# Kernel tuning notes

Measured on AMD Instinct MI355X. Metric: run time of the kernel, lower is better.

The kernel has to match this reference:

```python
import jax, jax.numpy as jnp
import numpy as np

N = 10000
E = 160000
DIMS = [512, 512, 512, 256]  # in -> hidden -> hidden -> out (num_layers=3)
EPS = 1e-12  # F.normalize default eps


def _sage_layer(x, edge_index, Wl, b, Wr):
    # PyG SAGEConv (mean aggr, normalize=True):
    # out = lin_l(mean_{j in N(i)} x_j) + lin_r(x_i), then L2-normalize rows.
    src = edge_index[0]
    dst = edge_index[1]
    msg = x[src]  # [E, d] gather of source-node features
    agg = jax.ops.segment_sum(msg, dst, num_segments=N)  # [N, d]
    cnt = jax.ops.segment_sum(jnp.ones((E,), x.dtype), dst, num_segments=N)
    mean = agg / jnp.maximum(cnt, 1.0)[:, None]
    out = mean @ Wl.T + b + x @ Wr.T
    norm = jnp.sqrt(jnp.sum(out * out, axis=-1, keepdims=True))
    return out / jnp.maximum(norm, EPS)


def setup_inputs() -> dict:
    key = jax.random.key(0)
    ks = jax.random.split(key, 2 + 3 * len(DIMS))
    x = jax.random.normal(ks[0], (N, DIMS[0]), dtype=jnp.float32)
    edge_index = jax.random.randint(ks[1], (2, E), 0, N, dtype=jnp.int64)
    inp = {"x": x, "edge_index": edge_index}
    k = 2
    for i in range(len(DIMS) - 1):
        din, dout = DIMS[i], DIMS[i + 1]
        s = 1.0 / np.sqrt(din)
        inp[f"Wl{i}"] = jax.random.uniform(ks[k], (dout, din), jnp.float32, -s, s); k += 1
        inp[f"b{i}"] = jax.random.uniform(ks[k], (dout,), jnp.float32, -s, s); k += 1
        inp[f"Wr{i}"] = jax.random.uniform(ks[k], (dout, din), jnp.float32, -s, s); k += 1
    return inp


def reference(x, edge_index, Wl0, b0, Wr0, Wl1, b1, Wr1, Wl2, b2, Wr2):
    params = [(Wl0, b0, Wr0), (Wl1, b1, Wr1), (Wl2, b2, Wr2)]
    for Wl, b, Wr in params:
        x = _sage_layer(x, edge_index, Wl, b, Wr)
        x = jax.nn.relu(x)
        # F.dropout(training=False) is identity at inference
    return x
```

## Files before the change

### kernel.cpp

```cpp
#include <hip/hip_runtime.h>

#define NN 10000

typedef __attribute__((ext_vector_type(8))) short short8;
typedef __attribute__((ext_vector_type(4))) float f32x4;

__device__ __forceinline__ ushort f2b(float f) {
    union { float f; uint32_t u; } v; v.f = f;
    uint32_t u = v.u;
    return (ushort)((u + 0x7fffu + ((u >> 16) & 1u)) >> 16);
}
__device__ __forceinline__ uint packbf(float a, float b) {
    return (uint)f2b(a) | ((uint)f2b(b) << 16);
}
__device__ __forceinline__ float blo(uint u) {
    union { uint u; float f; } v; v.u = u << 16; return v.f;
}
__device__ __forceinline__ float bhi(uint u) {
    union { uint u; float f; } v; v.u = u & 0xffff0000u; return v.f;
}

__global__ __launch_bounds__(256) void zero_int(int* __restrict__ p, int n) {
    int i = blockIdx.x * 256 + threadIdx.x;
    if (i < n) p[i] = 0;
}

__global__ __launch_bounds__(256) void count_dst(const int* __restrict__ dst,
                                                 int* __restrict__ counts, int E) {
    int i = blockIdx.x * 256 + threadIdx.x;
    if (i < E) atomicAdd(&counts[dst[i]], 1);
}

__global__ __launch_bounds__(1024) void scan_build(const int* __restrict__ counts,
                                                   int* __restrict__ offsets,
                                                   int* __restrict__ cursor,
                                                   float* __restrict__ inv_cnt, int n) {
    __shared__ int part[1024];
    int tid = threadIdx.x;
    int per = (n + 1023) / 1024;
    int base = tid * per;
    int s = 0;
    for (int i = 0; i < per; i++) { int idx = base + i; if (idx < n) s += counts[idx]; }
    part[tid] = s;
    __syncthreads();
    for (int off = 1; off < 1024; off <<= 1) {
        int v = (tid >= off) ? part[tid - off] : 0;
        __syncthreads();
        part[tid] += v;
        __syncthreads();
    }
    int run = (tid > 0) ? part[tid - 1] : 0;
    for (int i = 0; i < per; i++) {
        int idx = base + i;
        if (idx < n) {
            int c = counts[idx];
            offsets[idx] = run;
            cursor[idx]  = run;
            inv_cnt[idx] = 1.0f / fmaxf((float)c, 1.0f);
            run += c;
        }
    }
}

__global__ __launch_bounds__(256) void scatter_edges(const int* __restrict__ src,
                                                     const int* __restrict__ dst,
                                                     int* __restrict__ cursor,
                                                     int* __restrict__ sorted_src, int E) {
    int i = blockIdx.x * 256 + threadIdx.x;
    if (i < E) {
        int p = atomicAdd(&cursor[dst[i]], 1);
        sorted_src[p] = src[i];
    }
}

__global__ __launch_bounds__(256) void cvt_x(const float* __restrict__ in,
                                             ushort* __restrict__ xcat, int n4) {
    int i = blockIdx.x * 256 + threadIdx.x;
    if (i >= n4) return;
    int idx = i * 4;
    int node = idx >> 9;
    int col  = idx & 511;
    float4 v = *(const float4*)(in + (size_t)node * 512 + col);
    uint2 p;
    p.x = packbf(v.x, v.y);
    p.y = packbf(v.z, v.w);
    *(uint2*)(xcat + (size_t)node * 1024 + 512 + col) = p;
}

__global__ __launch_bounds__(256) void cvt_w(const float* __restrict__ Wl,
                                             const float* __restrict__ Wr,
                                             ushort* __restrict__ out, int n4) {
    int i = blockIdx.x * 256 + threadIdx.x;
    if (i >= n4) return;
    int idx = i * 4;
    int row = idx >> 10;
    int col = idx & 1023;
    const float* src = (col < 512) ? (Wl + (size_t)row * 512 + col)
                                   : (Wr + (size_t)row * 512 + col - 512);
    float4 v = *(const float4*)src;
    uint2 p;
    p.x = packbf(v.x, v.y);
    p.y = packbf(v.z, v.w);
    *(uint2*)(out + idx) = p;
}

__global__ __launch_bounds__(256) void agg_mean(ushort* __restrict__ xcat,
                                                const int* __restrict__ offsets,
                                                const int* __restrict__ counts,
                                                const int* __restrict__ sorted_src,
                                                const float* __restrict__ inv_cnt, int n) {
    int wave = threadIdx.x >> 6;
    int lane = threadIdx.x & 63;
    int node = blockIdx.x * 4 + wave;
    if (node >= n) return;
    int start = offsets[node];
    int cnt   = counts[node];
    float inv = inv_cnt[node];

    const uint* xr = (const uint*)xcat + 256;
    int l4 = lane * 4;

    float acc[8];
#pragma unroll
    for (int k = 0; k < 8; k++) acc[k] = 0.f;

    int e = 0;
    for (; e + 4 <= cnt; e += 4) {
        int s0 = sorted_src[start + e + 0];
        int s1 = sorted_src[start + e + 1];
        int s2 = sorted_src[start + e + 2];
        int s3 = sorted_src[start + e + 3];
        uint4 v0 = *(const uint4*)(xr + (size_t)s0 * 512 + l4);
        uint4 v1 = *(const uint4*)(xr + (size_t)s1 * 512 + l4);
        uint4 v2 = *(const uint4*)(xr + (size_t)s2 * 512 + l4);
        uint4 v3 = *(const uint4*)(xr + (size_t)s3 * 512 + l4);
#define ACC8(v) do { \
        acc[0] += blo(v.x); acc[1] += bhi(v.x); \
        acc[2] += blo(v.y); acc[3] += bhi(v.y); \
        acc[4] += blo(v.z); acc[5] += bhi(v.z); \
        acc[6] += blo(v.w); acc[7] += bhi(v.w); } while (0)
        ACC8(v0); ACC8(v1); ACC8(v2); ACC8(v3);
    }
    for (; e < cnt; e++) {
        int s0 = sorted_src[start + e];
        uint4 v0 = *(const uint4*)(xr + (size_t)s0 * 512 + l4);
        ACC8(v0);
    }
#undef ACC8

    uint4 o;
    o.x = packbf(acc[0] * inv, acc[1] * inv);
    o.y = packbf(acc[2] * inv, acc[3] * inv);
    o.z = packbf(acc[4] * inv, acc[5] * inv);
    o.w = packbf(acc[6] * inv, acc[7] * inv);
    *(uint4*)(xcat + (size_t)node * 1024 + lane * 8) = o;
}

__global__ __launch_bounds__(256) void gemm_mfma(const ushort* __restrict__ A,
                                                 const ushort* __restrict__ B,
                                                 float* __restrict__ C,
                                                 int M, int Nn) {
    __shared__ ushort Asl[64 * 32];
    __shared__ ushort Bsl[128 * 32];
    const int tid  = threadIdx.x;
    const int w    = tid >> 6;
    const int lane = tid & 63;
    const int bm = blockIdx.y * 64, bn = blockIdx.x * 128;
    const int wm = (w & 1) * 32, wn = (w >> 1) * 64;
    const int row16 = lane & 15, q = lane >> 4;

    f32x4 acc[2][4];
#pragma unroll
    for (int i = 0; i < 2; i++)
#pragma unroll
        for (int j = 0; j < 4; j++) acc[i][j] = (f32x4){0.f, 0.f, 0.f, 0.f};

    const int sc_r = lane >> 2;
    const int sc_s = lane & 3;
    const int koff = sc_s ^ ((sc_r >> 1) & 3);
    const int swz  = (row16 >> 1) & 3;

    for (int k0 = 0; k0 < 1024; k0 += 32) {
        {
            int rloc = w * 16 + sc_r;
            int grow = bm + rloc; grow = grow < M ? grow : M - 1;
            const ushort* gp = A + (size_t)grow * 1024 + k0 + koff * 8;
            __builtin_amdgcn_global_load_lds(
                (const __attribute__((address_space(1))) uint32_t*)gp,
                (__attribute__((address_space(3))) uint32_t*)&Asl[w * 512],
                16, 0, 0);
        }
#pragma unroll
        for (int c = 0; c < 2; c++) {
            int chunk = w * 2 + c;
            int rloc  = chunk * 16 + sc_r;
            const ushort* gp = B + (size_t)(bn + rloc) * 1024 + k0 + koff * 8;
            __builtin_amdgcn_global_load_lds(
                (const __attribute__((address_space(1))) uint32_t*)gp,
                (__attribute__((address_space(3))) uint32_t*)&Bsl[chunk * 512],
                16, 0, 0);
        }
        __syncthreads();

        short8 af[2], bfr[4];
        int s = q ^ swz;
#pragma unroll
        for (int i = 0; i < 2; i++) {
            int r = wm + i * 16 + row16;
            af[i] = *(const short8*)&Asl[r * 32 + s * 8];
        }
#pragma unroll
        for (int j = 0; j < 4; j++) {
            int rn = wn + j * 16 + row16;
            bfr[j] = *(const short8*)&Bsl[rn * 32 + s * 8];
        }
#pragma unroll
        for (int i = 0; i < 2; i++)
#pragma unroll
            for (int j = 0; j < 4; j++)
                acc[i][j] = __builtin_amdgcn_mfma_f32_16x16x32_bf16(
                    af[i], bfr[j], acc[i][j], 0, 0, 0);
        __syncthreads();
    }

#pragma unroll
    for (int i = 0; i < 2; i++) {
#pragma unroll
        for (int r2 = 0; r2 < 4; r2++) {
            int row = bm + wm + i * 16 + q * 4 + r2;
            if (row < M) {
                float* Cp = C + (size_t)row * Nn + bn + wn + row16;
#pragma unroll
                for (int j = 0; j < 4; j++)
                    Cp[j * 16] = acc[i][j][r2];
            }
        }
    }
}

template <int DOUT, bool FINAL>
__global__ __launch_bounds__(256) void finalize(const float* __restrict__ Cbuf,
                                                const float* __restrict__ bias,
                                                ushort* __restrict__ xcat,
                                                float* __restrict__ outf, int n) {
    const int PL = DOUT / 64;
    int wave = threadIdx.x >> 6;
    int lane = threadIdx.x & 63;
    int node = blockIdx.x * 4 + wave;
    if (node >= n) return;

    float v[PL];
    const float* Cp = Cbuf + (size_t)node * DOUT + lane * PL;
    const float* Bp = bias + lane * PL;
#pragma unroll
    for (int k = 0; k < PL; k += 4) {
        float4 c = *(const float4*)(Cp + k);
        float4 b = *(const float4*)(Bp + k);
        v[k + 0] = c.x + b.x; v[k + 1] = c.y + b.y;
        v[k + 2] = c.z + b.z; v[k + 3] = c.w + b.w;
    }
    float ss = 0.f;
#pragma unroll
    for (int k = 0; k < PL; k++) ss += v[k] * v[k];
#pragma unroll
    for (int m = 32; m >= 1; m >>= 1) ss += __shfl_xor(ss, m, 64);
    float scale = 1.0f / fmaxf(sqrtf(ss), 1e-12f);

    if (FINAL) {
        float* Op = outf + (size_t)node * DOUT + lane * PL;
#pragma unroll
        for (int k = 0; k < PL; k += 4) {
            float4 o;
            o.x = fmaxf(v[k + 0] * scale, 0.f);
            o.y = fmaxf(v[k + 1] * scale, 0.f);
            o.z = fmaxf(v[k + 2] * scale, 0.f);
            o.w = fmaxf(v[k + 3] * scale, 0.f);
            *(float4*)(Op + k) = o;
        }
    } else {
        uint4 o;
        float r0 = fmaxf(v[0] * scale, 0.f), r1 = fmaxf(v[1] * scale, 0.f);
        float r2 = fmaxf(v[2] * scale, 0.f), r3 = fmaxf(v[3] * scale, 0.f);
        float r4 = fmaxf(v[4] * scale, 0.f), r5 = fmaxf(v[5] * scale, 0.f);
        float r6 = fmaxf(v[6] * scale, 0.f), r7 = fmaxf(v[7] * scale, 0.f);
        o.x = packbf(r0, r1); o.y = packbf(r2, r3);
        o.z = packbf(r4, r5); o.w = packbf(r6, r7);
        *(uint4*)(xcat + (size_t)node * 1024 + 512 + lane * 8) = o;
    }
}

extern "C" void kernel_launch(void* const* d_in, const int* in_sizes, int n_in,
                              void* d_out, int out_size, void* d_ws, size_t ws_size,
                              hipStream_t stream) {
    const float* x    = (const float*)d_in[0];
    const int*   edge = (const int*)d_in[1];
    const float* Wl0  = (const float*)d_in[2];
    const float* b0   = (const float*)d_in[3];
    const float* Wr0  = (const float*)d_in[4];
    const float* Wl1  = (const float*)d_in[5];
    const float* b1   = (const float*)d_in[6];
    const float* Wr1  = (const float*)d_in[7];
    const float* Wl2  = (const float*)d_in[8];
    const float* b2   = (const float*)d_in[9];
    const float* Wr2  = (const float*)d_in[10];

    const int E = in_sizes[1] / 2;

    char* ws = (char*)d_ws;
    int*    counts  = (int*)(ws + 0);
    int*    offsets = (int*)(ws + 40960);
    int*    cursor  = (int*)(ws + 81920);
    float*  invc    = (float*)(ws + 122880);
    int*    sorted  = (int*)(ws + 163840);
    ushort* Wc0     = (ushort*)(ws + 804864);
    ushort* Wc1     = (ushort*)(ws + 1853440);
    ushort* Wc2     = (ushort*)(ws + 2902016);
    ushort* xcat    = (ushort*)(ws + 3426304);
    float*  Cbuf    = (float*)(ws + 23906304);

    zero_int<<<(NN + 255) / 256, 256, 0, stream>>>(counts, NN);
    count_dst<<<(E + 255) / 256, 256, 0, stream>>>(edge + E, counts, E);
    scan_build<<<1, 1024, 0, stream>>>(counts, offsets, cursor, invc, NN);
    scatter_edges<<<(E + 255) / 256, 256, 0, stream>>>(edge, edge + E, cursor, sorted, E);

    cvt_x<<<(NN * 512 / 4 + 255) / 256, 256, 0, stream>>>(x, xcat, NN * 512 / 4);
    cvt_w<<<(512 * 1024 / 4 + 255) / 256, 256, 0, stream>>>(Wl0, Wr0, Wc0, 512 * 1024 / 4);
    cvt_w<<<(512 * 1024 / 4 + 255) / 256, 256, 0, stream>>>(Wl1, Wr1, Wc1, 512 * 1024 / 4);
    cvt_w<<<(256 * 1024 / 4 + 255) / 256, 256, 0, stream>>>(Wl2, Wr2, Wc2, 256 * 1024 / 4);

    const int gyM = (NN + 63) / 64;
    const int gb  = (NN + 3) / 4;

    agg_mean<<<gb, 256, 0, stream>>>(xcat, offsets, counts, sorted, invc, NN);
    gemm_mfma<<<dim3(4, gyM), 256, 0, stream>>>(xcat, Wc0, Cbuf, NN, 512);
    finalize<512, false><<<gb, 256, 0, stream>>>(Cbuf, b0, xcat, nullptr, NN);
    agg_mean<<<gb, 256, 0, stream>>>(xcat, offsets, counts, sorted, invc, NN);
    gemm_mfma<<<dim3(4, gyM), 256, 0, stream>>>(xcat, Wc1, Cbuf, NN, 512);
    finalize<512, false><<<gb, 256, 0, stream>>>(Cbuf, b1, xcat, nullptr, NN);
    agg_mean<<<gb, 256, 0, stream>>>(xcat, offsets, counts, sorted, invc, NN);
    gemm_mfma<<<dim3(2, gyM), 256, 0, stream>>>(xcat, Wc2, Cbuf, NN, 256);
    finalize<256, true><<<gb, 256, 0, stream>>>(Cbuf, b2, nullptr, (float*)d_out, NN);
}
```

Measured before the change: 277.8 us.

## Transform before aggregate: GEMM x with stacked weights, then gather-mean projected rows

```diff
diff --git a/kernel.cpp b/kernel.cpp
--- a/kernel.cpp
+++ b/kernel.cpp
@@ -73,30 +73,29 @@
     }
 }
 
-__global__ __launch_bounds__(256) void cvt_x(const float* __restrict__ in,
-                                             ushort* __restrict__ xcat, int n4) {
+__global__ __launch_bounds__(256) void cvt_x2(const float* __restrict__ in,
+                                              ushort* __restrict__ out, int n4) {
     int i = blockIdx.x * 256 + threadIdx.x;
     if (i >= n4) return;
     int idx = i * 4;
-    int node = idx >> 9;
-    int col  = idx & 511;
-    float4 v = *(const float4*)(in + (size_t)node * 512 + col);
+    float4 v = *(const float4*)(in + idx);
     uint2 p;
     p.x = packbf(v.x, v.y);
     p.y = packbf(v.z, v.w);
-    *(uint2*)(xcat + (size_t)node * 1024 + 512 + col) = p;
-}
-
-__global__ __launch_bounds__(256) void cvt_w(const float* __restrict__ Wl,
-                                             const float* __restrict__ Wr,
-                                             ushort* __restrict__ out, int n4) {
+    *(uint2*)(out + idx) = p;
+}
+
+__global__ __launch_bounds__(256) void cvt_w2(const float* __restrict__ Wl,
+                                              const float* __restrict__ Wr,
+                                              ushort* __restrict__ out,
+                                              int dout, int n4) {
     int i = blockIdx.x * 256 + threadIdx.x;
     if (i >= n4) return;
     int idx = i * 4;
-    int row = idx >> 10;
-    int col = idx & 1023;
-    const float* src = (col < 512) ? (Wl + (size_t)row * 512 + col)
-                                   : (Wr + (size_t)row * 512 + col - 512);
+    int row = idx >> 9;
+    int col = idx & 511;
+    const float* src = (row < dout) ? (Wl + (size_t)row * 512 + col)
+                                    : (Wr + (size_t)(row - dout) * 512 + col);
     float4 v = *(const float4*)src;
     uint2 p;
     p.x = packbf(v.x, v.y);
@@ -104,11 +103,105 @@
     *(uint2*)(out + idx) = p;
 }
 
-__global__ __launch_bounds__(256) void agg_mean(ushort* __restrict__ xcat,
-                                                const int* __restrict__ offsets,
-                                                const int* __restrict__ counts,
-                                                const int* __restrict__ sorted_src,
-                                                const float* __restrict__ inv_cnt, int n) {
+__global__ __launch_bounds__(256) void gemm_split(const ushort* __restrict__ A,
+                                                  const ushort* __restrict__ B,
+                                                  ushort* __restrict__ G,
+                                                  float* __restrict__ R,
+                                                  int M, int dout) {
+    __shared__ ushort Asl[128 * 32];
+    __shared__ ushort Bsl[128 * 32];
+    const int tid  = threadIdx.x;
+    const int w    = tid >> 6;
+    const int lane = tid & 63;
+    const int bm = blockIdx.y * 128, bn = blockIdx.x * 128;
+    const int wm = (w & 1) * 64, wn = (w >> 1) * 64;
+    const int row16 = lane & 15, q = lane >> 4;
+
+    f32x4 acc[4][4];
+#pragma unroll
+    for (int i = 0; i < 4; i++)
+#pragma unroll
+        for (int j = 0; j < 4; j++) acc[i][j] = (f32x4){0.f, 0.f, 0.f, 0.f};
+
+    const int sc_r = lane >> 2;
+    const int sc_s = lane & 3;
+    const int koff = sc_s ^ ((sc_r >> 1) & 3);
+    const int swz  = (row16 >> 1) & 3;
+
+    for (int k0 = 0; k0 < 512; k0 += 32) {
+#pragma unroll
+        for (int c = 0; c < 2; c++) {
+            int chunk = w * 2 + c;
+            int rloc  = chunk * 16 + sc_r;
+            int growA = bm + rloc; growA = growA < M ? growA : M - 1;
+            const ushort* gpA = A + (size_t)growA * 512 + k0 + koff * 8;
+            __builtin_amdgcn_global_load_lds(
+                (const __attribute__((address_space(1))) uint32_t*)gpA,
+                (__attribute__((address_space(3))) uint32_t*)&Asl[chunk * 512],
+                16, 0, 0);
+            const ushort* gpB = B + (size_t)(bn + rloc) * 512 + k0 + koff * 8;
+            __builtin_amdgcn_global_load_lds(
+                (const __attribute__((address_space(1))) uint32_t*)gpB,
+                (__attribute__((address_space(3))) uint32_t*)&Bsl[chunk * 512],
+                16, 0, 0);
+        }
+        __syncthreads();
+
+        short8 af[4], bfr[4];
+        int s = q ^ swz;
+#pragma unroll
+        for (int i = 0; i < 4; i++) {
+            int r = wm + i * 16 + row16;
+            af[i] = *(const short8*)&Asl[r * 32 + s * 8];
+        }
+#pragma unroll
+        for (int j = 0; j < 4; j++) {
+            int rn = wn + j * 16 + row16;
+            bfr[j] = *(const short8*)&Bsl[rn * 32 + s * 8];
+        }
+#pragma unroll
+        for (int i = 0; i < 4; i++)
+#pragma unroll
+            for (int j = 0; j < 4; j++)
+                acc[i][j] = __builtin_amdgcn_mfma_f32_16x16x32_bf16(
+                    af[i], bfr[j], acc[i][j], 0, 0, 0);
+        __syncthreads();
+    }
+
+    const bool isR = (bn >= dout);
+#pragma unroll
+    for (int i = 0; i < 4; i++) {
+#pragma unroll
+        for (int r2 = 0; r2 < 4; r2++) {
+            int row = bm + wm + i * 16 + q * 4 + r2;
+            if (row < M) {
+                if (isR) {
+                    float* Rp = R + (size_t)row * dout + (bn - dout) + wn + row16;
+#pragma unroll
+                    for (int j = 0; j < 4; j++)
+                        Rp[j * 16] = acc[i][j][r2];
+                } else {
+                    ushort* Gp = G + (size_t)row * dout + bn + wn + row16;
+#pragma unroll
+                    for (int j = 0; j < 4; j++)
+                        Gp[j * 16] = f2b(acc[i][j][r2]);
+                }
+            }
+        }
+    }
+}
+
+template <int DOUT, bool FINAL>
+__global__ __launch_bounds__(256) void aggfin(const ushort* __restrict__ G,
+                                              const float* __restrict__ R,
+                                              const float* __restrict__ bias,
+                                              const int* __restrict__ offsets,
+                                              const int* __restrict__ counts,
+                                              const int* __restrict__ sorted_src,
+                                              const float* __restrict__ inv_cnt,
+                                              ushort* __restrict__ xnext,
+                                              float* __restrict__ outf, int n) {
+    constexpr int PL = DOUT / 64;
     int wave = threadIdx.x >> 6;
     int lane = threadIdx.x & 63;
     int node = blockIdx.x * 4 + wave;
@@ -117,147 +210,69 @@
     int cnt   = counts[node];
     float inv = inv_cnt[node];
 
-    const uint* xr = (const uint*)xcat + 256;
-    int l4 = lane * 4;
-
-    float acc[8];
-#pragma unroll
-    for (int k = 0; k < 8; k++) acc[k] = 0.f;
-
-    int e = 0;
-    for (; e + 4 <= cnt; e += 4) {
-        int s0 = sorted_src[start + e + 0];
-        int s1 = sorted_src[start + e + 1];
-        int s2 = sorted_src[start + e + 2];
-        int s3 = sorted_src[start + e + 3];
-        uint4 v0 = *(const uint4*)(xr + (size_t)s0 * 512 + l4);
-        uint4 v1 = *(const uint4*)(xr + (size_t)s1 * 512 + l4);
-        uint4 v2 = *(const uint4*)(xr + (size_t)s2 * 512 + l4);
-        uint4 v3 = *(const uint4*)(xr + (size_t)s3 * 512 + l4);
+    float acc[PL];
+#pragma unroll
+    for (int k = 0; k < PL; k++) acc[k] = 0.f;
+
+    if constexpr (DOUT == 512) {
+        const uint* gp = (const uint*)G + lane * 4;
 #define ACC8(v) do { \
         acc[0] += blo(v.x); acc[1] += bhi(v.x); \
         acc[2] += blo(v.y); acc[3] += bhi(v.y); \
         acc[4] += blo(v.z); acc[5] += bhi(v.z); \
         acc[6] += blo(v.w); acc[7] += bhi(v.w); } while (0)
-        ACC8(v0); ACC8(v1); ACC8(v2); ACC8(v3);
-    }
-    for (; e < cnt; e++) {
-        int s0 = sorted_src[start + e];
-        uint4 v0 = *(const uint4*)(xr + (size_t)s0 * 512 + l4);
-        ACC8(v0);
-    }
+        int e = 0;
+        for (; e + 8 <= cnt; e += 8) {
+            uint4 vv[8];
+#pragma unroll
+            for (int u = 0; u < 8; u++) {
+                int s0 = sorted_src[start + e + u];
+                vv[u] = *(const uint4*)(gp + (size_t)s0 * 256);
+            }
+#pragma unroll
+            for (int u = 0; u < 8; u++) ACC8(vv[u]);
+        }
+        for (; e < cnt; e++) {
+            int s0 = sorted_src[start + e];
+            uint4 v0 = *(const uint4*)(gp + (size_t)s0 * 256);
+            ACC8(v0);
+        }
 #undef ACC8
-
-    uint4 o;
-    o.x = packbf(acc[0] * inv, acc[1] * inv);
-    o.y = packbf(acc[2] * inv, acc[3] * inv);
-    o.z = packbf(acc[4] * inv, acc[5] * inv);
-    o.w = packbf(acc[6] * inv, acc[7] * inv);
-    *(uint4*)(xcat + (size_t)node * 1024 + lane * 8) = o;
-}
-
-__global__ __launch_bounds__(256) void gemm_mfma(const ushort* __restrict__ A,
-                                                 const ushort* __restrict__ B,
-                                                 float* __restrict__ C,
-                                                 int M, int Nn) {
-    __shared__ ushort Asl[64 * 32];
-    __shared__ ushort Bsl[128 * 32];
-    const int tid  = threadIdx.x;
-    const int w    = tid >> 6;
-    const int lane = tid & 63;
-    const int bm = blockIdx.y * 64, bn = blockIdx.x * 128;
-    const int wm = (w & 1) * 32, wn = (w >> 1) * 64;
-    const int row16 = lane & 15, q = lane >> 4;
-
-    f32x4 acc[2][4];
-#pragma unroll
-    for (int i = 0; i < 2; i++)
-#pragma unroll
-        for (int j = 0; j < 4; j++) acc[i][j] = (f32x4){0.f, 0.f, 0.f, 0.f};
-
-    const int sc_r = lane >> 2;
-    const int sc_s = lane & 3;
-    const int koff = sc_s ^ ((sc_r >> 1) & 3);
-    const int swz  = (row16 >> 1) & 3;
-
-    for (int k0 = 0; k0 < 1024; k0 += 32) {
-        {
-            int rloc = w * 16 + sc_r;
-            int grow = bm + rloc; grow = grow < M ? grow : M - 1;
-            const ushort* gp = A + (size_t)grow * 1024 + k0 + koff * 8;
-            __builtin_amdgcn_global_load_lds(
-                (const __attribute__((address_space(1))) uint32_t*)gp,
-                (__attribute__((address_space(3))) uint32_t*)&Asl[w * 512],
-                16, 0, 0);
-        }
-#pragma unroll
-        for (int c = 0; c < 2; c++) {
-            int chunk = w * 2 + c;
-            int rloc  = chunk * 16 + sc_r;
-            const ushort* gp = B + (size_t)(bn + rloc) * 1024 + k0 + koff * 8;
-            __builtin_amdgcn_global_load_lds(
-                (const __attribute__((address_space(1))) uint32_t*)gp,
-                (__attribute__((address_space(3))) uint32_t*)&Bsl[chunk * 512],
-                16, 0, 0);
-        }
-        __syncthreads();
-
-        short8 af[2], bfr[4];
-        int s = q ^ swz;
-#pragma unroll
-        for (int i = 0; i < 2; i++) {
-            int r = wm + i * 16 + row16;
-            af[i] = *(const short8*)&Asl[r * 32 + s * 8];
-        }
-#pragma unroll
-        for (int j = 0; j < 4; j++) {
-            int rn = wn + j * 16 + row16;
-            bfr[j] = *(const short8*)&Bsl[rn * 32 + s * 8];
-        }
-#pragma unroll
-        for (int i = 0; i < 2; i++)
-#pragma unroll
-            for (int j = 0; j < 4; j++)
-                acc[i][j] = __builtin_amdgcn_mfma_f32_16x16x32_bf16(
-                    af[i], bfr[j], acc[i][j], 0, 0, 0);
-        __syncthreads();
-    }
-
-#pragma unroll
-    for (int i = 0; i < 2; i++) {
-#pragma unroll
-        for (int r2 = 0; r2 < 4; r2++) {
-            int row = bm + wm + i * 16 + q * 4 + r2;
-            if (row < M) {
-                float* Cp = C + (size_t)row * Nn + bn + wn + row16;
-#pragma unroll
-                for (int j = 0; j < 4; j++)
-                    Cp[j * 16] = acc[i][j][r2];
+    } else {
+        const uint* gp = (const uint*)G + lane * 2;
+#define ACC4(v) do { \
+        acc[0] += blo(v.x); acc[1] += bhi(v.x); \
+        acc[2] += blo(v.y); acc[3] += bhi(v.y); } while (0)
+        int e = 0;
+        for (; e + 8 <= cnt; e += 8) {
+            uint2 vv[8];
+#pragma unroll
+            for (int u = 0; u < 8; u++) {
+                int s0 = sorted_src[start + e + u];
+                vv[u] = *(const uint2*)(gp + (size_t)s0 * 128);
             }
-        }
-    }
-}
-
-template <int DOUT, bool FINAL>
-__global__ __launch_bounds__(256) void finalize(const float* __restrict__ Cbuf,
-                                                const float* __restrict__ bias,
-                                                ushort* __restrict__ xcat,
-                                                float* __restrict__ outf, int n) {
-    const int PL = DOUT / 64;
-    int wave = threadIdx.x >> 6;
-    int lane = threadIdx.x & 63;
-    int node = blockIdx.x * 4 + wave;
-    if (node >= n) return;
+#pragma unroll
+            for (int u = 0; u < 8; u++) ACC4(vv[u]);
+        }
+        for (; e < cnt; e++) {
+            int s0 = sorted_src[start + e];
+            uint2 v0 = *(const uint2*)(gp + (size_t)s0 * 128);
+            ACC4(v0);
+        }
+#undef ACC4
+    }
 
     float v[PL];
-    const float* Cp = Cbuf + (size_t)node * DOUT + lane * PL;
+    const float* Rp = R + (size_t)node * DOUT + lane * PL;
     const float* Bp = bias + lane * PL;
 #pragma unroll
     for (int k = 0; k < PL; k += 4) {
-        float4 c = *(const float4*)(Cp + k);
-        float4 b = *(const float4*)(Bp + k);
-        v[k + 0] = c.x + b.x; v[k + 1] = c.y + b.y;
-        v[k + 2] = c.z + b.z; v[k + 3] = c.w + b.w;
+        float4 r4 = *(const float4*)(Rp + k);
+        float4 b4 = *(const float4*)(Bp + k);
+        v[k + 0] = acc[k + 0] * inv + r4.x + b4.x;
+        v[k + 1] = acc[k + 1] * inv + r4.y + b4.y;
+        v[k + 2] = acc[k + 2] * inv + r4.z + b4.z;
+        v[k + 3] = acc[k + 3] * inv + r4.w + b4.w;
     }
     float ss = 0.f;
 #pragma unroll
@@ -266,7 +281,7 @@
     for (int m = 32; m >= 1; m >>= 1) ss += __shfl_xor(ss, m, 64);
     float scale = 1.0f / fmaxf(sqrtf(ss), 1e-12f);
 
-    if (FINAL) {
+    if constexpr (FINAL) {
         float* Op = outf + (size_t)node * DOUT + lane * PL;
 #pragma unroll
         for (int k = 0; k < PL; k += 4) {
@@ -285,7 +300,7 @@
         float r6 = fmaxf(v[6] * scale, 0.f), r7 = fmaxf(v[7] * scale, 0.f);
         o.x = packbf(r0, r1); o.y = packbf(r2, r3);
         o.z = packbf(r4, r5); o.w = packbf(r6, r7);
-        *(uint4*)(xcat + (size_t)node * 1024 + 512 + lane * 8) = o;
+        *(uint4*)(xnext + (size_t)node * 512 + lane * 8) = o;
     }
 }
 
@@ -312,32 +327,33 @@
     int*    cursor  = (int*)(ws + 81920);
     float*  invc    = (float*)(ws + 122880);
     int*    sorted  = (int*)(ws + 163840);
-    ushort* Wc0     = (ushort*)(ws + 804864);
-    ushort* Wc1     = (ushort*)(ws + 1853440);
-    ushort* Wc2     = (ushort*)(ws + 2902016);
-    ushort* xcat    = (ushort*)(ws + 3426304);
-    float*  Cbuf    = (float*)(ws + 23906304);
+    ushort* Wc0     = (ushort*)(ws + 819200);
+    ushort* Wc1     = (ushort*)(ws + 1867776);
+    ushort* Wc2     = (ushort*)(ws + 2916352);
+    ushort* xbuf    = (ushort*)(ws + 3440640);
+    ushort* Gbuf    = (ushort*)(ws + 13680640);
+    float*  Rbuf    = (float*)(ws + 23920640);
 
     zero_int<<<(NN + 255) / 256, 256, 0, stream>>>(counts, NN);
     count_dst<<<(E + 255) / 256, 256, 0, stream>>>(edge + E, counts, E);
     scan_build<<<1, 1024, 0, stream>>>(counts, offsets, cursor, invc, NN);
     scatter_edges<<<(E + 255) / 256, 256, 0, stream>>>(edge, edge + E, cursor, sorted, E);
 
-    cvt_x<<<(NN * 512 / 4 + 255) / 256, 256, 0, stream>>>(x, xcat, NN * 512 / 4);
-    cvt_w<<<(512 * 1024 / 4 + 255) / 256, 256, 0, stream>>>(Wl0, Wr0, Wc0, 512 * 1024 / 4);
-    cvt_w<<<(512 * 1024 / 4 + 255) / 256, 256, 0, stream>>>(Wl1, Wr1, Wc1, 512 * 1024 / 4);
-    cvt_w<<<(256 * 1024 / 4 + 255) / 256, 256, 0, stream>>>(Wl2, Wr2, Wc2, 256 * 1024 / 4);
-
-    const int gyM = (NN + 63) / 64;
+    cvt_x2<<<(NN * 512 / 4 + 255) / 256, 256, 0, stream>>>(x, xbuf, NN * 512 / 4);
+    cvt_w2<<<(1024 * 512 / 4 + 255) / 256, 256, 0, stream>>>(Wl0, Wr0, Wc0, 512, 1024 * 512 / 4);
+    cvt_w2<<<(1024 * 512 / 4 + 255) / 256, 256, 0, stream>>>(Wl1, Wr1, Wc1, 512, 1024 * 512 / 4);
+    cvt_w2<<<(512 * 512 / 4 + 255) / 256, 256, 0, stream>>>(Wl2, Wr2, Wc2, 256, 512 * 512 / 4);
+
+    const int gyM = (NN + 127) / 128;
     const int gb  = (NN + 3) / 4;
 
-    agg_mean<<<gb, 256, 0, stream>>>(xcat, offsets, counts, sorted, invc, NN);
-    gemm_mfma<<<dim3(4, gyM), 256, 0, stream>>>(xcat, Wc0, Cbuf, NN, 512);
-    finalize<512, false><<<gb, 256, 0, stream>>>(Cbuf, b0, xcat, nullptr, NN);
-    agg_mean<<<gb, 256, 0, stream>>>(xcat, offsets, counts, sorted, invc, NN);
-    gemm_mfma<<<dim3(4, gyM), 256, 0, stream>>>(xcat, Wc1, Cbuf, NN, 512);
-    finalize<512, false><<<gb, 256, 0, stream>>>(Cbuf, b1, xcat, nullptr, NN);
-    agg_mean<<<gb, 256, 0, stream>>>(xcat, offsets, counts, sorted, invc, NN);
-    gemm_mfma<<<dim3(2, gyM), 256, 0, stream>>>(xcat, Wc2, Cbuf, NN, 256);
-    finalize<256, true><<<gb, 256, 0, stream>>>(Cbuf, b2, nullptr, (float*)d_out, NN);
-}
+    gemm_split<<<dim3(8, gyM), 256, 0, stream>>>(xbuf, Wc0, Gbuf, Rbuf, NN, 512);
+    aggfin<512, false><<<gb, 256, 0, stream>>>(Gbuf, Rbuf, b0, offsets, counts,
+                                               sorted, invc, xbuf, nullptr, NN);
+    gemm_split<<<dim3(8, gyM), 256, 0, stream>>>(xbuf, Wc1, Gbuf, Rbuf, NN, 512);
+    aggfin<512, false><<<gb, 256, 0, stream>>>(Gbuf, Rbuf, b1, offsets, counts,
+                                               sorted, invc, xbuf, nullptr, NN);
+    gemm_split<<<dim3(4, gyM), 256, 0, stream>>>(xbuf, Wc2, Gbuf, Rbuf, NN, 256);
+    aggfin<256, true><<<gb, 256, 0, stream>>>(Gbuf, Rbuf, b2, offsets, counts,
+                                              sorted, invc, nullptr, (float*)d_out, NN);
+}
```

New measurement: 275.1 us. About the same (-1.0%).
